# Kernel optimization log

Measured on AMD Instinct MI355X. Metric: run time of the kernel, lower is better.

## Reference

```python
import jax, jax.numpy as jnp
import numpy as np

N_NODES = 100000
N_EDGES = 1600000
IN, HID, OUT = 128, 128, 64


def setup_inputs() -> dict:
    key = jax.random.key(0)
    ks = jax.random.split(key, 12)
    x = jax.random.normal(ks[0], (N_NODES, IN), dtype=jnp.float32)
    src = jax.random.randint(ks[1], (N_EDGES,), 0, N_NODES, dtype=jnp.int32)
    dst = jax.random.randint(ks[2], (N_EDGES,), 0, N_NODES, dtype=jnp.int32)

    def lin(k, fan_in, fan_out):
        return jax.random.normal(k, (fan_in, fan_out), dtype=jnp.float32) / jnp.sqrt(jnp.float32(fan_in))

    return {
        "x": x, "src": src, "dst": dst,
        "w_self_0": lin(ks[3], IN, HID), "w_neigh_0": lin(ks[4], IN, HID), "b_0": jnp.zeros((HID,), jnp.float32),
        "w_self_1": lin(ks[5], HID, HID), "w_neigh_1": lin(ks[6], HID, HID), "b_1": jnp.zeros((HID,), jnp.float32),
        "w_self_2": lin(ks[7], HID, OUT), "w_neigh_2": lin(ks[8], HID, OUT), "b_2": jnp.zeros((OUT,), jnp.float32),
    }


def reference(x, src, dst, w_self_0, w_neigh_0, b_0, w_self_1, w_neigh_1, b_1, w_self_2, w_neigh_2, b_2):
    n = x.shape[0]
    # in-degree per dst node; zero-degree nodes keep aggregated 0 (clamp avoids div-by-0)
    deg = jax.ops.segment_sum(jnp.ones_like(dst, dtype=x.dtype), dst, num_segments=n)
    inv_deg = (1.0 / jnp.maximum(deg, 1.0))[:, None]

    def sage_layer(h, w_s, w_n, b):
        # irregular gather of src features, segment-mean over dst
        agg = jax.ops.segment_sum(h[src], dst, num_segments=n) * inv_deg
        return h @ w_s + agg @ w_n + b

    h = jax.nn.relu(sage_layer(x, w_self_0, w_neigh_0, b_0))   # dropout = identity (eval)
    h = jax.nn.relu(sage_layer(h, w_self_1, w_neigh_1, b_1))
    return sage_layer(h, w_self_2, w_neigh_2, b_2)
```

## Files before the change

kernel.cpp:

```cpp
#include <hip/hip_runtime.h>


#define NN 100000
#define NE 1600000
#define BSH 7
#define BND 128
#define NB  782
#define NBLKS 256
#define EPB ((NE + NBLKS - 1) / NBLKS)
#define STOT (NB * NBLKS)
#define NSB ((STOT + 1023) / 1024)
#define GEMM_BLOCKS 1563

typedef __attribute__((ext_vector_type(8))) short short8;
typedef __attribute__((ext_vector_type(4))) float f32x4;
typedef unsigned int uint;
typedef unsigned short ushort;

__device__ inline ushort f2bf(float f) {
    uint u = __float_as_uint(f);
    u += 0x7FFFu + ((u >> 16) & 1u);
    return (ushort)(u >> 16);
}
__device__ inline float bf_lo(uint w) { return __uint_as_float(w << 16); }
__device__ inline float bf_hi(uint w) { return __uint_as_float(w & 0xFFFF0000u); }

template<int NCS, int NCN, bool XF32, bool ABF>
__device__ void gemm_body(int bid, int tid,
    const void* __restrict__ Hv, const ushort* __restrict__ Wf,
    const float* __restrict__ bias, void* __restrict__ Av, ushort* __restrict__ Bt)
{
    constexpr int NCT = (NCS + NCN) / 16;
    const int g = (bid * 256 + tid) >> 6;
    if (g >= NN / 16) return;
    const int lane = tid & 63;
    const int m = lane & 15;
    const int q = lane >> 4;

    short8 af[4];
    if (XF32) {
        const float* hp = (const float*)Hv + (size_t)(g * 16 + m) * 128;
        #pragma unroll
        for (int kt = 0; kt < 4; ++kt) {
            const float4 f0 = *(const float4*)(hp + kt * 32 + q * 8);
            const float4 f1 = *(const float4*)(hp + kt * 32 + q * 8 + 4);
            short8 v;
            v[0] = (short)f2bf(f0.x); v[1] = (short)f2bf(f0.y);
            v[2] = (short)f2bf(f0.z); v[3] = (short)f2bf(f0.w);
            v[4] = (short)f2bf(f1.x); v[5] = (short)f2bf(f1.y);
            v[6] = (short)f2bf(f1.z); v[7] = (short)f2bf(f1.w);
            af[kt] = v;
        }
    } else {
        const short8* hp = (const short8*)((const ushort*)Hv + (size_t)(g * 16 + m) * 128);
        #pragma unroll
        for (int kt = 0; kt < 4; ++kt) af[kt] = hp[kt * 4 + q];
    }

    f32x4 acc[NCT];
    #pragma unroll
    for (int i = 0; i < NCT; ++i) acc[i] = (f32x4){0.f, 0.f, 0.f, 0.f};

    const short8* wp = (const short8*)Wf;
    #pragma unroll
    for (int ct = 0; ct < NCT; ++ct) {
        #pragma unroll
        for (int kt = 0; kt < 4; ++kt) {
            const short8 bf = wp[(ct * 4 + kt) * 64 + lane];
            acc[ct] = __builtin_amdgcn_mfma_f32_16x16x32_bf16(af[kt], bf, acc[ct], 0, 0, 0);
        }
    }

    const int r0 = g * 16 + q * 4;
    #pragma unroll
    for (int ct = 0; ct < NCS / 16; ++ct) {
        const int c = ct * 16 + m;
        const float bv = bias[c];
        #pragma unroll
        for (int r = 0; r < 4; ++r) {
            const float v = acc[ct][r] + bv;
            if (ABF) ((ushort*)Av)[(size_t)(r0 + r) * NCS + c] = f2bf(v);
            else     ((float*) Av)[(size_t)(r0 + r) * NCS + c] = v;
        }
    }
    #pragma unroll
    for (int ct = NCS / 16; ct < NCT; ++ct) {
        const int c = ct * 16 + m - NCS;
        #pragma unroll
        for (int r = 0; r < 4; ++r)
            Bt[(size_t)(r0 + r) * NCN + c] = f2bf(acc[ct][r]);
    }
}

template<int NCS, int NCN, bool XF32, bool ABF>
__global__ __launch_bounds__(256) void gemm_mfma_k(
    const void* __restrict__ Hv, const ushort* __restrict__ Wf,
    const float* __restrict__ bias, void* __restrict__ Av, ushort* __restrict__ Bt)
{
    gemm_body<NCS, NCN, XF32, ABF>(blockIdx.x, threadIdx.x, Hv, Wf, bias, Av, Bt);
}

__global__ __launch_bounds__(256) void phist_pack_k(
    const int* __restrict__ dst, int* __restrict__ histG,
    const float* __restrict__ ws0, const float* __restrict__ wn0, ushort* __restrict__ wf0,
    const float* __restrict__ ws1, const float* __restrict__ wn1, ushort* __restrict__ wf1,
    const float* __restrict__ ws2, const float* __restrict__ wn2, ushort* __restrict__ wf2)
{
    __shared__ int h[NB];
    const int t = threadIdx.x;
    if (blockIdx.x < NBLKS) {
        for (int i = t; i < NB; i += 256) h[i] = 0;
        __syncthreads();
        const int blk = blockIdx.x;
        const int e0 = blk * EPB;
        const int e1 = min(e0 + EPB, NE);
        for (int e = e0 + t; e < e1; e += 256)
            atomicAdd(&h[dst[e] >> BSH], 1);
        __syncthreads();
        for (int i = t; i < NB; i += 256)
            histG[i * NBLKS + blk] = h[i];
        return;
    }
    const int b = blockIdx.x - NBLKS;
    const float *ws, *wn; ushort* wf; int ncs, idx;
    if (b < 16)      { ws = ws0; wn = wn0; wf = wf0; ncs = 128; idx = b * 256 + t; }
    else if (b < 32) { ws = ws1; wn = wn1; wf = wf1; ncs = 128; idx = (b - 16) * 256 + t; }
    else             { ws = ws2; wn = wn2; wf = wf2; ncs = 64;  idx = (b - 32) * 256 + t; }
    const int total = (2 * ncs / 16) * 4 * 64;
    if (idx >= total) return;
    const int l = idx & 63;
    const int f = idx >> 6;
    const int kt = f & 3;
    const int ct = f >> 2;
    const int n = ct * 16 + (l & 15);
    const int k0 = kt * 32 + (l >> 4) * 8;
    uint w[4];
    #pragma unroll
    for (int p = 0; p < 4; ++p) {
        const int k = k0 + p * 2;
        float v0, v1;
        if (n < ncs) { v0 = ws[k * ncs + n];         v1 = ws[(k + 1) * ncs + n]; }
        else         { v0 = wn[k * ncs + (n - ncs)]; v1 = wn[(k + 1) * ncs + (n - ncs)]; }
        w[p] = (uint)f2bf(v0) | ((uint)f2bf(v1) << 16);
    }
    uint4 o; o.x = w[0]; o.y = w[1]; o.z = w[2]; o.w = w[3];
    ((uint4*)wf)[idx] = o;
}

__global__ __launch_bounds__(256) void scan1_k(int* __restrict__ data, int* __restrict__ blksum) {
    __shared__ int lds[256];
    const int t = threadIdx.x;
    const int base = blockIdx.x * 1024 + t * 4;
    int v[4];
    #pragma unroll
    for (int i = 0; i < 4; ++i) {
        const int idx = base + i;
        v[i] = (idx < STOT) ? data[idx] : 0;
    }
    const int s = v[0] + v[1] + v[2] + v[3];
    lds[t] = s;
    __syncthreads();
    #pragma unroll
    for (int off = 1; off < 256; off <<= 1) {
        const int cur = lds[t];
        const int y = (t >= off) ? lds[t - off] : 0;
        __syncthreads();
        lds[t] = cur + y;
        __syncthreads();
    }
    const int incl = lds[t];
    if (t == 255) blksum[blockIdx.x] = incl;
    int run = incl - s;
    #pragma unroll
    for (int i = 0; i < 4; ++i) {
        const int idx = base + i;
        if (idx < STOT) data[idx] = run;
        run += v[i];
    }
}

__global__ __launch_bounds__(256) void scan3_k(int* __restrict__ data, const int* __restrict__ blksum) {
    __shared__ int lds[256];
    const int t = threadIdx.x;
    lds[t] = (t < NSB) ? blksum[t] : 0;
    __syncthreads();
    #pragma unroll
    for (int off = 1; off < 256; off <<= 1) {
        const int cur = lds[t];
        const int y = (t >= off) ? lds[t - off] : 0;
        __syncthreads();
        lds[t] = cur + y;
        __syncthreads();
    }
    const int add = (blockIdx.x == 0) ? 0 : lds[blockIdx.x - 1];
    const int base = blockIdx.x * 1024 + t * 4;
    #pragma unroll
    for (int i = 0; i < 4; ++i) {
        const int idx = base + i;
        if (idx < STOT) data[idx] += add;
    }
}

__global__ __launch_bounds__(256) void pscatter_gemm0_k(
    const int* __restrict__ src, const int* __restrict__ dst,
    const int* __restrict__ histG, int* __restrict__ pb,
    const float* __restrict__ x, const ushort* __restrict__ wf0,
    const float* __restrict__ b0, ushort* __restrict__ Abf, ushort* __restrict__ Bt)
{
    __shared__ int wc[NB];
    const int t = threadIdx.x;
    if (blockIdx.x < NBLKS) {
        const int blk = blockIdx.x;
        for (int i = t; i < NB; i += 256) wc[i] = histG[i * NBLKS + blk];
        __syncthreads();
        const int e0 = blk * EPB;
        const int e1 = min(e0 + EPB, NE);
        for (int e = e0 + t; e < e1; e += 256) {
            const int d = dst[e];
            const int pos = atomicAdd(&wc[d >> BSH], 1);
            pb[pos] = (src[e] << BSH) | (d & (BND - 1));
        }
        return;
    }
    gemm_body<128, 128, true, true>(blockIdx.x - NBLKS, t, x, wf0, b0, Abf, Bt);
}

__global__ __launch_bounds__(256) void bucket_place_k(const int* __restrict__ histG,
                                                      const int* __restrict__ pb,
                                                      int* __restrict__ row,
                                                      int* __restrict__ esrc) {
    __shared__ int cnt[BND], wc[BND], excl[BND], scan[BND];
    const int b = blockIdx.x;
    const int t = threadIdx.x;
    if (t < BND) { cnt[t] = 0; wc[t] = 0; }
    __syncthreads();
    const int s0 = histG[b * NBLKS];
    const int s1 = (b + 1 < NB) ? histG[(b + 1) * NBLKS] : NE;
    for (int e = s0 + t; e < s1; e += 256)
        atomicAdd(&cnt[pb[e] & (BND - 1)], 1);
    __syncthreads();
    if (t < BND) scan[t] = cnt[t];
    __syncthreads();
    for (int off = 1; off < BND; off <<= 1) {
        int nv = 0;
        if (t < BND) {
            nv = scan[t];
            if (t >= off) nv += scan[t - off];
        }
        __syncthreads();
        if (t < BND) scan[t] = nv;
        __syncthreads();
    }
    if (t < BND) {
        const int ex = scan[t] - cnt[t];
        excl[t] = ex;
        const int node = b * BND + t;
        if (node <= NN) row[node] = s0 + ex;
    }
    __syncthreads();
    for (int e = s0 + t; e < s1; e += 256) {
        const int p = pb[e];
        const int dl = p & (BND - 1);
        const int pos = s0 + excl[dl] + atomicAdd(&wc[dl], 1);
        esrc[pos] = p >> BSH;
    }
}

__global__ __launch_bounds__(256) void agg128_k(
    const int* __restrict__ row, const int* __restrict__ esrc,
    const ushort* __restrict__ Bt, const ushort* __restrict__ Abf, ushort* __restrict__ Hb)
{
    const int w = (blockIdx.x * 256 + threadIdx.x) >> 6;
    const int half = (threadIdx.x >> 5) & 1;
    const int ln = threadIdx.x & 31;
    const int node = w * 2 + half;
    if (node >= NN) return;
    const int e0 = row[node];
    const int e1 = row[node + 1];
    const uint2* B = (const uint2*)Bt;
    float a0 = 0.f, a1 = 0.f, a2 = 0.f, a3 = 0.f;
    int e = e0;
    for (; e + 8 <= e1; e += 8) {
        int s[8];
        #pragma unroll
        for (int j = 0; j < 8; ++j) s[j] = esrc[e + j];
        uint2 v[8];
        #pragma unroll
        for (int j = 0; j < 8; ++j) v[j] = B[(size_t)s[j] * 32 + ln];
        #pragma unroll
        for (int j = 0; j < 8; ++j) {
            a0 += bf_lo(v[j].x); a1 += bf_hi(v[j].x);
            a2 += bf_lo(v[j].y); a3 += bf_hi(v[j].y);
        }
    }
    for (; e + 2 <= e1; e += 2) {
        const int s0 = esrc[e], s1 = esrc[e + 1];
        const uint2 v0 = B[(size_t)s0 * 32 + ln];
        const uint2 v1 = B[(size_t)s1 * 32 + ln];
        a0 += bf_lo(v0.x) + bf_lo(v1.x); a1 += bf_hi(v0.x) + bf_hi(v1.x);
        a2 += bf_lo(v0.y) + bf_lo(v1.y); a3 += bf_hi(v0.y) + bf_hi(v1.y);
    }
    if (e < e1) {
        const uint2 v = B[(size_t)esrc[e] * 32 + ln];
        a0 += bf_lo(v.x); a1 += bf_hi(v.x);
        a2 += bf_lo(v.y); a3 += bf_hi(v.y);
    }
    const int deg = e1 - e0;
    const float invd = (deg > 0) ? 1.0f / (float)deg : 0.0f;
    const uint2 aw = ((const uint2*)Abf)[(size_t)node * 32 + ln];
    const float v0 = fmaxf(bf_lo(aw.x) + a0 * invd, 0.f);
    const float v1 = fmaxf(bf_hi(aw.x) + a1 * invd, 0.f);
    const float v2 = fmaxf(bf_lo(aw.y) + a2 * invd, 0.f);
    const float v3 = fmaxf(bf_hi(aw.y) + a3 * invd, 0.f);
    uint2 o;
    o.x = (uint)f2bf(v0) | ((uint)f2bf(v1) << 16);
    o.y = (uint)f2bf(v2) | ((uint)f2bf(v3) << 16);
    ((uint2*)Hb)[(size_t)node * 32 + ln] = o;
}

__global__ __launch_bounds__(256) void agg64_k(
    const int* __restrict__ row, const int* __restrict__ esrc,
    const ushort* __restrict__ Bt, float* __restrict__ out)
{
    const int node = (blockIdx.x * 256 + threadIdx.x) >> 4;
    const int ln = threadIdx.x & 15;
    if (node >= NN) return;
    const int e0 = row[node];
    const int e1 = row[node + 1];
    const uint2* B = (const uint2*)Bt;
    float a0 = 0.f, a1 = 0.f, a2 = 0.f, a3 = 0.f;
    int e = e0;
    for (; e + 8 <= e1; e += 8) {
        int s[8];
        #pragma unroll
        for (int j = 0; j < 8; ++j) s[j] = esrc[e + j];
        uint2 v[8];
        #pragma unroll
        for (int j = 0; j < 8; ++j) v[j] = B[(size_t)s[j] * 16 + ln];
        #pragma unroll
        for (int j = 0; j < 8; ++j) {
            a0 += bf_lo(v[j].x); a1 += bf_hi(v[j].x);
            a2 += bf_lo(v[j].y); a3 += bf_hi(v[j].y);
        }
    }
    for (; e + 2 <= e1; e += 2) {
        const int s0 = esrc[e], s1 = esrc[e + 1];
        const uint2 v0 = B[(size_t)s0 * 16 + ln];
        const uint2 v1 = B[(size_t)s1 * 16 + ln];
        a0 += bf_lo(v0.x) + bf_lo(v1.x); a1 += bf_hi(v0.x) + bf_hi(v1.x);
        a2 += bf_lo(v0.y) + bf_lo(v1.y); a3 += bf_hi(v0.y) + bf_hi(v1.y);
    }
    if (e < e1) {
        const uint2 v = B[(size_t)esrc[e] * 16 + ln];
        a0 += bf_lo(v.x); a1 += bf_hi(v.x);
        a2 += bf_lo(v.y); a3 += bf_hi(v.y);
    }
    const int deg = e1 - e0;
    const float invd = (deg > 0) ? 1.0f / (float)deg : 0.0f;
    float4* op = (float4*)(out + (size_t)node * 64 + ln * 4);
    float4 o = *op;
    o.x += a0 * invd; o.y += a1 * invd;
    o.z += a2 * invd; o.w += a3 * invd;
    *op = o;
}

__device__ inline float4 relu4f(float4 v) {
    v.x = fmaxf(v.x, 0.f); v.y = fmaxf(v.y, 0.f);
    v.z = fmaxf(v.z, 0.f); v.w = fmaxf(v.w, 0.f);
    return v;
}
template<int NCOL, bool RELU_IN, bool BIAS>
__global__ __launch_bounds__(256) void gemm_k(
    const float* in, const float* __restrict__ W,
    const float* __restrict__ bias, float* out)
{
    constexpr int K = 128;
    constexpr int QUADS = NCOL / 4;
    constexpr int G = 256 / QUADS;
    constexpr int RPT = 32 / G;
    __shared__ float Wlds[K * NCOL];
    {
        const float4* Wg = reinterpret_cast<const float4*>(W);
        float4* Wl = reinterpret_cast<float4*>(Wlds);
        #pragma unroll
        for (int i = 0; i < K * NCOL / 4 / 256; ++i)
            Wl[threadIdx.x + i * 256] = Wg[threadIdx.x + i * 256];
    }
    __syncthreads();
    const int tx = threadIdx.x % QUADS;
    const int ty = threadIdx.x / QUADS;
    const int row0 = blockIdx.x * 32;
    const float* rp[RPT];
    #pragma unroll
    for (int i = 0; i < RPT; ++i) rp[i] = in + (size_t)(row0 + ty + i * G) * K;
    float acc[RPT][4];
    #pragma unroll
    for (int i = 0; i < RPT; ++i) acc[i][0] = acc[i][1] = acc[i][2] = acc[i][3] = 0.f;
    #pragma unroll 2
    for (int kc = 0; kc < K; kc += 4) {
        float4 h4[RPT];
        #pragma unroll
        for (int i = 0; i < RPT; ++i) {
            h4[i] = *reinterpret_cast<const float4*>(rp[i] + kc);
            if (RELU_IN) h4[i] = relu4f(h4[i]);
        }
        #pragma unroll
        for (int kk = 0; kk < 4; ++kk) {
            const float4 w4 = *reinterpret_cast<const float4*>(&Wlds[(kc + kk) * NCOL + tx * 4]);
            #pragma unroll
            for (int i = 0; i < RPT; ++i) {
                const float hv = (&h4[i].x)[kk];
                acc[i][0] = fmaf(hv, w4.x, acc[i][0]);
                acc[i][1] = fmaf(hv, w4.y, acc[i][1]);
                acc[i][2] = fmaf(hv, w4.z, acc[i][2]);
                acc[i][3] = fmaf(hv, w4.w, acc[i][3]);
            }
        }
    }
    float4 b4 = make_float4(0.f, 0.f, 0.f, 0.f);
    if (BIAS) b4 = *reinterpret_cast<const float4*>(&bias[tx * 4]);
    #pragma unroll
    for (int i = 0; i < RPT; ++i) {
        const int r = row0 + ty + i * G;
        float4 o;
        o.x = acc[i][0] + b4.x; o.y = acc[i][1] + b4.y;
        o.z = acc[i][2] + b4.z; o.w = acc[i][3] + b4.w;
        *reinterpret_cast<float4*>(&out[(size_t)r * NCOL + tx * 4]) = o;
    }
}
__global__ void deg_k(const int* __restrict__ dst, float* __restrict__ deg, int E) {
    const int i = blockIdx.x * blockDim.x + threadIdx.x;
    if (i < E) atomicAdd(&deg[dst[i]], 1.0f);
}
__global__ void inv_k(float* deg, int n) {
    const int i = blockIdx.x * blockDim.x + threadIdx.x;
    if (i < n) deg[i] = 1.0f / fmaxf(deg[i], 1.0f);
}
__global__ __launch_bounds__(256) void scatter128_k(
    const int* __restrict__ src, const int* __restrict__ dst,
    const float* __restrict__ inv, const float* __restrict__ B, float* A, int E) {
    const int lane = threadIdx.x & 63;
    int w = (blockIdx.x * 256 + threadIdx.x) >> 6;
    const int nw = (gridDim.x * 256) >> 6;
    for (int e = w; e < E; e += nw) {
        const int s = src[e], d = dst[e];
        const float sc = inv[d];
        const float2 v = *reinterpret_cast<const float2*>(&B[(size_t)s * 128 + lane * 2]);
        atomicAdd(&A[(size_t)d * 128 + lane * 2    ], v.x * sc);
        atomicAdd(&A[(size_t)d * 128 + lane * 2 + 1], v.y * sc);
    }
}
__global__ __launch_bounds__(256) void scatter64_k(
    const int* __restrict__ src, const int* __restrict__ dst,
    const float* __restrict__ inv, const float* __restrict__ B, float* A, int E) {
    const int lane = threadIdx.x & 63;
    int w = (blockIdx.x * 256 + threadIdx.x) >> 6;
    const int nw = (gridDim.x * 256) >> 6;
    for (int e = w; e < E; e += nw) {
        const int s = src[e], d = dst[e];
        atomicAdd(&A[(size_t)d * 64 + lane], B[(size_t)s * 64 + lane] * inv[d]);
    }
}

extern "C" void kernel_launch(void* const* d_in, const int* in_sizes, int n_in,
                              void* d_out, int out_size, void* d_ws, size_t ws_size,
                              hipStream_t stream) {
    const float* x   = (const float*)d_in[0];
    const int*   src = (const int*)  d_in[1];
    const int*   dst = (const int*)  d_in[2];
    const float* ws0 = (const float*)d_in[3];
    const float* wn0 = (const float*)d_in[4];
    const float* b0  = (const float*)d_in[5];
    const float* ws1 = (const float*)d_in[6];
    const float* wn1 = (const float*)d_in[7];
    const float* b1  = (const float*)d_in[8];
    const float* ws2 = (const float*)d_in[9];
    const float* wn2 = (const float*)d_in[10];
    const float* b2  = (const float*)d_in[11];
    float* out = (float*)d_out;

    const size_t O_BLK  = 4096;
    const size_t O_ROW  = 16384;
    const size_t O_WF0  = 417792;
    const size_t O_WF1  = 483328;
    const size_t O_WF2  = 548864;
    const size_t O_ESRC = 581632;
    const size_t O_PB   = 6983680;
    const size_t O_HIST = 13385728;
    const size_t O_A    = 14286848;
    const size_t O_BT   = 39890944;
    const size_t O_HB   = 65495040;
    const size_t NEED   = 91095040;

    if (ws_size >= NEED) {
        int*    blks  = (int*)   ((char*)d_ws + O_BLK);
        int*    row   = (int*)   ((char*)d_ws + O_ROW);
        ushort* wf0   = (ushort*)((char*)d_ws + O_WF0);
        ushort* wf1   = (ushort*)((char*)d_ws + O_WF1);
        ushort* wf2   = (ushort*)((char*)d_ws + O_WF2);
        int*    esrc  = (int*)   ((char*)d_ws + O_ESRC);
        int*    pb    = (int*)   ((char*)d_ws + O_PB);
        int*    histG = (int*)   ((char*)d_ws + O_HIST);
        ushort* Abf   = (ushort*)((char*)d_ws + O_A);
        ushort* Bt    = (ushort*)((char*)d_ws + O_BT);
        ushort* Hb    = (ushort*)((char*)d_ws + O_HB);

        phist_pack_k<<<NBLKS + 40, 256, 0, stream>>>(dst, histG,
            ws0, wn0, wf0, ws1, wn1, wf1, ws2, wn2, wf2);
        scan1_k<<<NSB, 256, 0, stream>>>(histG, blks);
        scan3_k<<<NSB, 256, 0, stream>>>(histG, blks);
        pscatter_gemm0_k<<<NBLKS + GEMM_BLOCKS, 256, 0, stream>>>(
            src, dst, histG, pb, x, wf0, b0, Abf, Bt);
        bucket_place_k<<<NB, 256, 0, stream>>>(histG, pb, row, esrc);

        const int AGG128_BLOCKS = (NN / 2 + 3) / 4;
        const int AGG64_BLOCKS  = (NN + 63) / 64;
        const int A64B = (NN + 15) / 16;

        agg128_k<<<AGG128_BLOCKS, 256, 0, stream>>>(row, esrc, Bt, Abf, Hb);
        gemm_mfma_k<128, 128, false, true ><<<GEMM_BLOCKS, 256, 0, stream>>>(Hb, wf1, b1, Abf, Bt);
        agg128_k<<<AGG128_BLOCKS, 256, 0, stream>>>(row, esrc, Bt, Abf, Hb);
        gemm_mfma_k<64, 64, false, false><<<GEMM_BLOCKS, 256, 0, stream>>>(Hb, wf2, b2, out, Bt);
        agg64_k<<<A64B, 256, 0, stream>>>(row, esrc, Bt, out);
        (void)AGG64_BLOCKS;
    } else {
        float* inv = (float*)d_ws;
        float* H0  = (float*)((char*)d_ws + (1u << 20));
        float* Bf  = H0 + (size_t)NN * 128;
        const int GB = NN / 32;
        const int SC_BLOCKS = 4096;
        hipMemsetAsync(inv, 0, NN * sizeof(float), stream);
        deg_k<<<(NE + 255) / 256, 256, 0, stream>>>(dst, inv, NE);
        inv_k<<<(NN + 255) / 256, 256, 0, stream>>>(inv, NN);
        gemm_k<128, false, false><<<GB, 256, 0, stream>>>(x, wn0, nullptr, Bf);
        gemm_k<128, false, true ><<<GB, 256, 0, stream>>>(x, ws0, b0, H0);
        scatter128_k<<<SC_BLOCKS, 256, 0, stream>>>(src, dst, inv, Bf, H0, NE);
        gemm_k<128, true, false><<<GB, 256, 0, stream>>>(H0, wn1, nullptr, Bf);
        gemm_k<128, true, true ><<<GB, 256, 0, stream>>>(H0, ws1, b1, H0);
        scatter128_k<<<SC_BLOCKS, 256, 0, stream>>>(src, dst, inv, Bf, H0, NE);
        gemm_k<64, true, false><<<GB, 256, 0, stream>>>(H0, wn2, nullptr, Bf);
        gemm_k<64, true, true ><<<GB, 256, 0, stream>>>(H0, ws2, b2, out);
        scatter64_k<<<SC_BLOCKS, 256, 0, stream>>>(src, dst, inv, Bf, out, NE);
    }
}
```

Baseline: 397.5 us.

## Fuse edge histogram and local scan into scatter kernel, drop global scan passes

Each scatter block now builds its own dst-bucket histogram, runs a local prefix scan, and writes edges into its own slice of the partition buffer. Per-bucket totals are accumulated with global atomics, and bucket_place_k derives its start offset by reducing those totals. This removes the separate histogram kernel and the two global scan kernels. The cost is that bucket_place_k reads each of 256 per-block segments serially per thread, so loads are uncoalesced and the work per thread is uneven. It also adds a memset and atomics on the totals.

```diff
diff --git a/kernel.cpp b/kernel.cpp
--- a/kernel.cpp
+++ b/kernel.cpp
@@ -7,9 +7,7 @@
 #define BND 128
 #define NB  782
 #define NBLKS 256
-#define EPB ((NE + NBLKS - 1) / NBLKS)
-#define STOT (NB * NBLKS)
-#define NSB ((STOT + 1023) / 1024)
+#define EPB (NE / NBLKS)
 #define GEMM_BLOCKS 1563
 
 typedef __attribute__((ext_vector_type(8))) short short8;
@@ -25,103 +23,13 @@
 __device__ inline float bf_lo(uint w) { return __uint_as_float(w << 16); }
 __device__ inline float bf_hi(uint w) { return __uint_as_float(w & 0xFFFF0000u); }
 
-template<int NCS, int NCN, bool XF32, bool ABF>
-__device__ void gemm_body(int bid, int tid,
-    const void* __restrict__ Hv, const ushort* __restrict__ Wf,
-    const float* __restrict__ bias, void* __restrict__ Av, ushort* __restrict__ Bt)
-{
-    constexpr int NCT = (NCS + NCN) / 16;
-    const int g = (bid * 256 + tid) >> 6;
-    if (g >= NN / 16) return;
-    const int lane = tid & 63;
-    const int m = lane & 15;
-    const int q = lane >> 4;
-
-    short8 af[4];
-    if (XF32) {
-        const float* hp = (const float*)Hv + (size_t)(g * 16 + m) * 128;
-        #pragma unroll
-        for (int kt = 0; kt < 4; ++kt) {
-            const float4 f0 = *(const float4*)(hp + kt * 32 + q * 8);
-            const float4 f1 = *(const float4*)(hp + kt * 32 + q * 8 + 4);
-            short8 v;
-            v[0] = (short)f2bf(f0.x); v[1] = (short)f2bf(f0.y);
-            v[2] = (short)f2bf(f0.z); v[3] = (short)f2bf(f0.w);
-            v[4] = (short)f2bf(f1.x); v[5] = (short)f2bf(f1.y);
-            v[6] = (short)f2bf(f1.z); v[7] = (short)f2bf(f1.w);
-            af[kt] = v;
-        }
-    } else {
-        const short8* hp = (const short8*)((const ushort*)Hv + (size_t)(g * 16 + m) * 128);
-        #pragma unroll
-        for (int kt = 0; kt < 4; ++kt) af[kt] = hp[kt * 4 + q];
-    }
-
-    f32x4 acc[NCT];
-    #pragma unroll
-    for (int i = 0; i < NCT; ++i) acc[i] = (f32x4){0.f, 0.f, 0.f, 0.f};
-
-    const short8* wp = (const short8*)Wf;
-    #pragma unroll
-    for (int ct = 0; ct < NCT; ++ct) {
-        #pragma unroll
-        for (int kt = 0; kt < 4; ++kt) {
-            const short8 bf = wp[(ct * 4 + kt) * 64 + lane];
-            acc[ct] = __builtin_amdgcn_mfma_f32_16x16x32_bf16(af[kt], bf, acc[ct], 0, 0, 0);
-        }
-    }
-
-    const int r0 = g * 16 + q * 4;
-    #pragma unroll
-    for (int ct = 0; ct < NCS / 16; ++ct) {
-        const int c = ct * 16 + m;
-        const float bv = bias[c];
-        #pragma unroll
-        for (int r = 0; r < 4; ++r) {
-            const float v = acc[ct][r] + bv;
-            if (ABF) ((ushort*)Av)[(size_t)(r0 + r) * NCS + c] = f2bf(v);
-            else     ((float*) Av)[(size_t)(r0 + r) * NCS + c] = v;
-        }
-    }
-    #pragma unroll
-    for (int ct = NCS / 16; ct < NCT; ++ct) {
-        const int c = ct * 16 + m - NCS;
-        #pragma unroll
-        for (int r = 0; r < 4; ++r)
-            Bt[(size_t)(r0 + r) * NCN + c] = f2bf(acc[ct][r]);
-    }
-}
-
-template<int NCS, int NCN, bool XF32, bool ABF>
-__global__ __launch_bounds__(256) void gemm_mfma_k(
-    const void* __restrict__ Hv, const ushort* __restrict__ Wf,
-    const float* __restrict__ bias, void* __restrict__ Av, ushort* __restrict__ Bt)
-{
-    gemm_body<NCS, NCN, XF32, ABF>(blockIdx.x, threadIdx.x, Hv, Wf, bias, Av, Bt);
-}
-
-__global__ __launch_bounds__(256) void phist_pack_k(
-    const int* __restrict__ dst, int* __restrict__ histG,
+__global__ __launch_bounds__(256) void pack_k(
     const float* __restrict__ ws0, const float* __restrict__ wn0, ushort* __restrict__ wf0,
     const float* __restrict__ ws1, const float* __restrict__ wn1, ushort* __restrict__ wf1,
     const float* __restrict__ ws2, const float* __restrict__ wn2, ushort* __restrict__ wf2)
 {
-    __shared__ int h[NB];
+    const int b = blockIdx.x;
     const int t = threadIdx.x;
-    if (blockIdx.x < NBLKS) {
-        for (int i = t; i < NB; i += 256) h[i] = 0;
-        __syncthreads();
-        const int blk = blockIdx.x;
-        const int e0 = blk * EPB;
-        const int e1 = min(e0 + EPB, NE);
-        for (int e = e0 + t; e < e1; e += 256)
-            atomicAdd(&h[dst[e] >> BSH], 1);
-        __syncthreads();
-        for (int i = t; i < NB; i += 256)
-            histG[i * NBLKS + blk] = h[i];
-        return;
-    }
-    const int b = blockIdx.x - NBLKS;
     const float *ws, *wn; ushort* wf; int ncs, idx;
     if (b < 16)      { ws = ws0; wn = wn0; wf = wf0; ncs = 128; idx = b * 256 + t; }
     else if (b < 32) { ws = ws1; wn = wn1; wf = wf1; ncs = 128; idx = (b - 16) * 256 + t; }
@@ -147,97 +55,166 @@
     ((uint4*)wf)[idx] = o;
 }
 
-__global__ __launch_bounds__(256) void scan1_k(int* __restrict__ data, int* __restrict__ blksum) {
-    __shared__ int lds[256];
-    const int t = threadIdx.x;
-    const int base = blockIdx.x * 1024 + t * 4;
-    int v[4];
-    #pragma unroll
-    for (int i = 0; i < 4; ++i) {
-        const int idx = base + i;
-        v[i] = (idx < STOT) ? data[idx] : 0;
-    }
-    const int s = v[0] + v[1] + v[2] + v[3];
-    lds[t] = s;
-    __syncthreads();
-    #pragma unroll
-    for (int off = 1; off < 256; off <<= 1) {
-        const int cur = lds[t];
-        const int y = (t >= off) ? lds[t - off] : 0;
-        __syncthreads();
-        lds[t] = cur + y;
-        __syncthreads();
-    }
-    const int incl = lds[t];
-    if (t == 255) blksum[blockIdx.x] = incl;
-    int run = incl - s;
-    #pragma unroll
-    for (int i = 0; i < 4; ++i) {
-        const int idx = base + i;
-        if (idx < STOT) data[idx] = run;
-        run += v[i];
-    }
-}
-
-__global__ __launch_bounds__(256) void scan3_k(int* __restrict__ data, const int* __restrict__ blksum) {
-    __shared__ int lds[256];
-    const int t = threadIdx.x;
-    lds[t] = (t < NSB) ? blksum[t] : 0;
-    __syncthreads();
-    #pragma unroll
-    for (int off = 1; off < 256; off <<= 1) {
-        const int cur = lds[t];
-        const int y = (t >= off) ? lds[t - off] : 0;
-        __syncthreads();
-        lds[t] = cur + y;
-        __syncthreads();
-    }
-    const int add = (blockIdx.x == 0) ? 0 : lds[blockIdx.x - 1];
-    const int base = blockIdx.x * 1024 + t * 4;
-    #pragma unroll
-    for (int i = 0; i < 4; ++i) {
-        const int idx = base + i;
-        if (idx < STOT) data[idx] += add;
-    }
+template<int NCS, int NCN, bool XF32, bool ABF>
+__device__ void gemm_body(int bid, int tid,
+    const void* __restrict__ Hv, const ushort* __restrict__ Wf,
+    const float* __restrict__ bias, void* __restrict__ Av, ushort* __restrict__ Bt)
+{
+    constexpr int NCT = (NCS + NCN) / 16;
+    const int g = (bid * 256 + tid) >> 6;
+    if (g >= NN / 16) return;
+    const int lane = tid & 63;
+    const int m = lane & 15;
+    const int q = lane >> 4;
+
+    short8 af[4];
+    if (XF32) {
+        const float* hp = (const float*)Hv + (size_t)(g * 16 + m) * 128;
+        #pragma unroll
+        for (int kt = 0; kt < 4; ++kt) {
+            const float4 f0 = *(const float4*)(hp + kt * 32 + q * 8);
+            const float4 f1 = *(const float4*)(hp + kt * 32 + q * 8 + 4);
+            short8 v;
+            v[0] = (short)f2bf(f0.x); v[1] = (short)f2bf(f0.y);
+            v[2] = (short)f2bf(f0.z); v[3] = (short)f2bf(f0.w);
+            v[4] = (short)f2bf(f1.x); v[5] = (short)f2bf(f1.y);
+            v[6] = (short)f2bf(f1.z); v[7] = (short)f2bf(f1.w);
+            af[kt] = v;
+        }
+    } else {
+        const short8* hp = (const short8*)((const ushort*)Hv + (size_t)(g * 16 + m) * 128);
+        #pragma unroll
+        for (int kt = 0; kt < 4; ++kt) af[kt] = hp[kt * 4 + q];
+    }
+
+    f32x4 acc[NCT];
+    #pragma unroll
+    for (int i = 0; i < NCT; ++i) acc[i] = (f32x4){0.f, 0.f, 0.f, 0.f};
+
+    const short8* wp = (const short8*)Wf;
+    #pragma unroll
+    for (int ct = 0; ct < NCT; ++ct) {
+        #pragma unroll
+        for (int kt = 0; kt < 4; ++kt) {
+            const short8 bf = wp[(ct * 4 + kt) * 64 + lane];
+            acc[ct] = __builtin_amdgcn_mfma_f32_16x16x32_bf16(af[kt], bf, acc[ct], 0, 0, 0);
+        }
+    }
+
+    const int r0 = g * 16 + q * 4;
+    #pragma unroll
+    for (int ct = 0; ct < NCS / 16; ++ct) {
+        const int c = ct * 16 + m;
+        const float bv = bias[c];
+        #pragma unroll
+        for (int r = 0; r < 4; ++r) {
+            const float v = acc[ct][r] + bv;
+            if (ABF) ((ushort*)Av)[(size_t)(r0 + r) * NCS + c] = f2bf(v);
+            else     ((float*) Av)[(size_t)(r0 + r) * NCS + c] = v;
+        }
+    }
+    #pragma unroll
+    for (int ct = NCS / 16; ct < NCT; ++ct) {
+        const int c = ct * 16 + m - NCS;
+        #pragma unroll
+        for (int r = 0; r < 4; ++r)
+            Bt[(size_t)(r0 + r) * NCN + c] = f2bf(acc[ct][r]);
+    }
+}
+
+template<int NCS, int NCN, bool XF32, bool ABF>
+__global__ __launch_bounds__(256) void gemm_mfma_k(
+    const void* __restrict__ Hv, const ushort* __restrict__ Wf,
+    const float* __restrict__ bias, void* __restrict__ Av, ushort* __restrict__ Bt)
+{
+    gemm_body<NCS, NCN, XF32, ABF>(blockIdx.x, threadIdx.x, Hv, Wf, bias, Av, Bt);
 }
 
 __global__ __launch_bounds__(256) void pscatter_gemm0_k(
     const int* __restrict__ src, const int* __restrict__ dst,
-    const int* __restrict__ histG, int* __restrict__ pb,
+    int* __restrict__ pb, int* __restrict__ lofs, int* __restrict__ btot,
     const float* __restrict__ x, const ushort* __restrict__ wf0,
     const float* __restrict__ b0, ushort* __restrict__ Abf, ushort* __restrict__ Bt)
 {
+    __shared__ int h[NB];
     __shared__ int wc[NB];
+    __shared__ int tsum[256];
     const int t = threadIdx.x;
-    if (blockIdx.x < NBLKS) {
-        const int blk = blockIdx.x;
-        for (int i = t; i < NB; i += 256) wc[i] = histG[i * NBLKS + blk];
+    if (blockIdx.x >= NBLKS) {
+        gemm_body<128, 128, true, true>(blockIdx.x - NBLKS, t, x, wf0, b0, Abf, Bt);
+        return;
+    }
+    const int blk = blockIdx.x;
+    const int e0 = blk * EPB;
+    for (int i = t; i < NB; i += 256) h[i] = 0;
+    __syncthreads();
+    for (int e = e0 + t; e < e0 + EPB; e += 256)
+        atomicAdd(&h[dst[e] >> BSH], 1);
+    __syncthreads();
+    int v[4];
+    const int base4 = t * 4;
+    #pragma unroll
+    for (int i = 0; i < 4; ++i) {
+        const int idx = base4 + i;
+        v[i] = (idx < NB) ? h[idx] : 0;
+    }
+    const int s = v[0] + v[1] + v[2] + v[3];
+    tsum[t] = s;
+    __syncthreads();
+    #pragma unroll
+    for (int off = 1; off < 256; off <<= 1) {
+        const int cur = tsum[t];
+        const int y = (t >= off) ? tsum[t - off] : 0;
         __syncthreads();
-        const int e0 = blk * EPB;
-        const int e1 = min(e0 + EPB, NE);
-        for (int e = e0 + t; e < e1; e += 256) {
-            const int d = dst[e];
-            const int pos = atomicAdd(&wc[d >> BSH], 1);
-            pb[pos] = (src[e] << BSH) | (d & (BND - 1));
-        }
-        return;
-    }
-    gemm_body<128, 128, true, true>(blockIdx.x - NBLKS, t, x, wf0, b0, Abf, Bt);
-}
-
-__global__ __launch_bounds__(256) void bucket_place_k(const int* __restrict__ histG,
-                                                      const int* __restrict__ pb,
-                                                      int* __restrict__ row,
-                                                      int* __restrict__ esrc) {
+        tsum[t] = cur + y;
+        __syncthreads();
+    }
+    int run = tsum[t] - s;
+    #pragma unroll
+    for (int i = 0; i < 4; ++i) {
+        const int idx = base4 + i;
+        if (idx < NB) {
+            wc[idx] = run;
+            lofs[idx * NBLKS + blk] = run;
+            if (v[i]) atomicAdd(&btot[idx], v[i]);
+        }
+        run += v[i];
+    }
+    __syncthreads();
+    for (int e = e0 + t; e < e0 + EPB; e += 256) {
+        const int d = dst[e];
+        const int pos = e0 + atomicAdd(&wc[d >> BSH], 1);
+        pb[pos] = (src[e] << BSH) | (d & (BND - 1));
+    }
+}
+
+__global__ __launch_bounds__(256) void bucket_place_k(
+    const int* __restrict__ btot, const int* __restrict__ lofs,
+    const int* __restrict__ pb, int* __restrict__ row, int* __restrict__ esrc)
+{
     __shared__ int cnt[BND], wc[BND], excl[BND], scan[BND];
+    __shared__ int red[256];
     const int b = blockIdx.x;
     const int t = threadIdx.x;
+    int part = 0;
+    #pragma unroll
+    for (int i = 0; i < 4; ++i) {
+        const int idx = t * 4 + i;
+        if (idx < b && idx < NB) part += btot[idx];
+    }
+    red[t] = part;
     if (t < BND) { cnt[t] = 0; wc[t] = 0; }
     __syncthreads();
-    const int s0 = histG[b * NBLKS];
-    const int s1 = (b + 1 < NB) ? histG[(b + 1) * NBLKS] : NE;
-    for (int e = s0 + t; e < s1; e += 256)
-        atomicAdd(&cnt[pb[e] & (BND - 1)], 1);
+    for (int off = 128; off > 0; off >>= 1) {
+        if (t < off) red[t] += red[t + off];
+        __syncthreads();
+    }
+    const int s0 = red[0];
+    const int lo = lofs[b * NBLKS + t];
+    const int lcount = ((b + 1 < NB) ? lofs[(b + 1) * NBLKS + t] : EPB) - lo;
+    const int lstart = t * EPB + lo;
+    for (int k = 0; k < lcount; ++k)
+        atomicAdd(&cnt[pb[lstart + k] & (BND - 1)], 1);
     __syncthreads();
     if (t < BND) scan[t] = cnt[t];
     __syncthreads();
@@ -258,8 +235,8 @@
         if (node <= NN) row[node] = s0 + ex;
     }
     __syncthreads();
-    for (int e = s0 + t; e < s1; e += 256) {
-        const int p = pb[e];
+    for (int k = 0; k < lcount; ++k) {
+        const int p = pb[lstart + k];
         const int dl = p & (BND - 1);
         const int pos = s0 + excl[dl] + atomicAdd(&wc[dl], 1);
         esrc[pos] = p >> BSH;
@@ -479,42 +456,39 @@
     const float* b2  = (const float*)d_in[11];
     float* out = (float*)d_out;
 
-    const size_t O_BLK  = 4096;
+    const size_t O_BTOT = 4096;
     const size_t O_ROW  = 16384;
     const size_t O_WF0  = 417792;
     const size_t O_WF1  = 483328;
     const size_t O_WF2  = 548864;
     const size_t O_ESRC = 581632;
     const size_t O_PB   = 6983680;
-    const size_t O_HIST = 13385728;
-    const size_t O_A    = 14286848;
-    const size_t O_BT   = 39890944;
-    const size_t O_HB   = 65495040;
-    const size_t NEED   = 91095040;
+    const size_t O_LOFS = 13383680;
+    const size_t O_A    = 14185472;
+    const size_t O_BT   = 39785472;
+    const size_t O_HB   = 65385472;
+    const size_t NEED   = 90985472;
 
     if (ws_size >= NEED) {
-        int*    blks  = (int*)   ((char*)d_ws + O_BLK);
-        int*    row   = (int*)   ((char*)d_ws + O_ROW);
-        ushort* wf0   = (ushort*)((char*)d_ws + O_WF0);
-        ushort* wf1   = (ushort*)((char*)d_ws + O_WF1);
-        ushort* wf2   = (ushort*)((char*)d_ws + O_WF2);
-        int*    esrc  = (int*)   ((char*)d_ws + O_ESRC);
-        int*    pb    = (int*)   ((char*)d_ws + O_PB);
-        int*    histG = (int*)   ((char*)d_ws + O_HIST);
-        ushort* Abf   = (ushort*)((char*)d_ws + O_A);
-        ushort* Bt    = (ushort*)((char*)d_ws + O_BT);
-        ushort* Hb    = (ushort*)((char*)d_ws + O_HB);
-
-        phist_pack_k<<<NBLKS + 40, 256, 0, stream>>>(dst, histG,
-            ws0, wn0, wf0, ws1, wn1, wf1, ws2, wn2, wf2);
-        scan1_k<<<NSB, 256, 0, stream>>>(histG, blks);
-        scan3_k<<<NSB, 256, 0, stream>>>(histG, blks);
+        int*    btot = (int*)   ((char*)d_ws + O_BTOT);
+        int*    row  = (int*)   ((char*)d_ws + O_ROW);
+        ushort* wf0  = (ushort*)((char*)d_ws + O_WF0);
+        ushort* wf1  = (ushort*)((char*)d_ws + O_WF1);
+        ushort* wf2  = (ushort*)((char*)d_ws + O_WF2);
+        int*    esrc = (int*)   ((char*)d_ws + O_ESRC);
+        int*    pb   = (int*)   ((char*)d_ws + O_PB);
+        int*    lofs = (int*)   ((char*)d_ws + O_LOFS);
+        ushort* Abf  = (ushort*)((char*)d_ws + O_A);
+        ushort* Bt   = (ushort*)((char*)d_ws + O_BT);
+        ushort* Hb   = (ushort*)((char*)d_ws + O_HB);
+
+        hipMemsetAsync(btot, 0, NB * sizeof(int), stream);
+        pack_k<<<40, 256, 0, stream>>>(ws0, wn0, wf0, ws1, wn1, wf1, ws2, wn2, wf2);
         pscatter_gemm0_k<<<NBLKS + GEMM_BLOCKS, 256, 0, stream>>>(
-            src, dst, histG, pb, x, wf0, b0, Abf, Bt);
-        bucket_place_k<<<NB, 256, 0, stream>>>(histG, pb, row, esrc);
+            src, dst, pb, lofs, btot, x, wf0, b0, Abf, Bt);
+        bucket_place_k<<<NB, 256, 0, stream>>>(btot, lofs, pb, row, esrc);
 
         const int AGG128_BLOCKS = (NN / 2 + 3) / 4;
-        const int AGG64_BLOCKS  = (NN + 63) / 64;
         const int A64B = (NN + 15) / 16;
 
         agg128_k<<<AGG128_BLOCKS, 256, 0, stream>>>(row, esrc, Bt, Abf, Hb);
@@ -522,7 +496,6 @@
         agg128_k<<<AGG128_BLOCKS, 256, 0, stream>>>(row, esrc, Bt, Abf, Hb);
         gemm_mfma_k<64, 64, false, false><<<GEMM_BLOCKS, 256, 0, stream>>>(Hb, wf2, b2, out, Bt);
         agg64_k<<<A64B, 256, 0, stream>>>(row, esrc, Bt, out);
-        (void)AGG64_BLOCKS;
     } else {
         float* inv = (float*)d_ws;
         float* H0  = (float*)((char*)d_ws + (1u << 20));
```

Result: slower. 416.0 us (+4.7%).
